# Performance work log

Measured on AMD Instinct MI355X. Metric: run time of the kernel, lower is better.

Reference implementation:

```python
import jax, jax.numpy as jnp
import numpy as np

N, E, B = 10000, 160000, 64
H, M, NE = 64, 64, 10
NIN = NE + 1
L = 16  # (max_ell+1)^2 spherical-harmonic components, max_ell=3
NUM_LAYERS = 2
AVG_NEIGH = 16.0
NORM = 4.0  # normalization_factor
EPS = 1e-9

silu = jax.nn.silu


def sph_harm(u):
    # component-normalized real spherical harmonics l=0..3 of unit vectors u [E,3]
    x, y, z = u[..., 0], u[..., 1], u[..., 2]
    xx, yy, zz = x * x, y * y, z * z
    return jnp.stack([
        jnp.ones_like(x),
        1.7320508 * x, 1.7320508 * y, 1.7320508 * z,
        3.8729833 * x * y, 3.8729833 * y * z, 1.1180340 * (3.0 * zz - 1.0),
        3.8729833 * x * z, 1.9364917 * (xx - yy),
        2.0916500 * y * (3.0 * xx - yy), 10.2469508 * x * y * z,
        1.6201852 * y * (5.0 * zz - 1.0), 1.3228757 * z * (5.0 * zz - 3.0),
        1.6201852 * x * (5.0 * zz - 1.0), 5.1234754 * (xx - yy) * z,
        2.0916500 * x * (xx - 3.0 * yy),
    ], axis=-1)


def setup_inputs() -> dict:
    key = jax.random.key(0)
    ks = jax.random.split(key, 24)
    inp = {}
    inp["positions"] = jax.random.normal(ks[0], (N, 3), jnp.float32) * 3.0
    inp["node_attrs"] = jax.random.uniform(ks[1], (N, NE), jnp.float32)
    inp["t"] = jax.random.uniform(ks[2], (B, 1), jnp.float32)
    inp["shifts"] = jnp.zeros((E, 3), jnp.float32)
    inp["batch"] = jnp.sort(jax.random.randint(ks[3], (N,), 0, B))
    inp["edge_index"] = jax.random.randint(ks[4], (2, E), 0, N)

    def w(k, shape, fan_in):
        return (jax.random.normal(k, shape, jnp.float32) / np.float32(np.sqrt(fan_in)))

    inp["W_emb"] = w(ks[5], (NIN, H), NIN)
    inp["b_emb"] = jnp.zeros((H,), jnp.float32)
    inp["W_out"] = w(ks[6], (H, NIN), H)
    inp["b_out"] = jnp.zeros((NIN,), jnp.float32)
    inp["Wr1"] = w(ks[7], (NUM_LAYERS, 1, H), 1)
    inp["br1"] = jnp.zeros((NUM_LAYERS, H), jnp.float32)
    inp["Wr2"] = w(ks[8], (NUM_LAYERS, H, H), H)
    inp["W_up"] = w(ks[9], (NUM_LAYERS, H, H), H)
    inp["W_mix"] = w(ks[10], (NUM_LAYERS, H, H), H)
    inp["W_prod"] = w(ks[11], (NUM_LAYERS, H, H), H)
    inp["Wro1"] = w(ks[12], (NUM_LAYERS, H, M), H)
    inp["bro1"] = jnp.zeros((NUM_LAYERS, M), jnp.float32)
    inp["Wro2"] = w(ks[13], (NUM_LAYERS, M, H), M)
    inp["Wg"] = w(ks[14], (NUM_LAYERS, H, H), H)
    inp["wv"] = w(ks[15], (NUM_LAYERS, H), H)
    inp["Wmlp1"] = w(ks[16], (NUM_LAYERS, 2 * H, H), 2 * H)
    inp["bmlp1"] = jnp.zeros((NUM_LAYERS, H), jnp.float32)
    inp["Wmlp2"] = w(ks[17], (NUM_LAYERS, H, H), H)
    inp["bmlp2"] = jnp.zeros((NUM_LAYERS, H), jnp.float32)
    return inp


def reference(positions, node_attrs, t, shifts, batch, edge_index,
              W_emb, b_emb, W_out, b_out,
              Wr1, br1, Wr2, W_up, W_mix, W_prod,
              Wro1, bro1, Wro2, Wg, wv,
              Wmlp1, bmlp1, Wmlp2, bmlp2):
    snd, rcv = edge_index[0], edge_index[1]

    def edges(p):
        v = p[rcv] - p[snd] + shifts          # [E,3]
        return v, jnp.linalg.norm(v, axis=-1, keepdims=True)

    na = node_attrs / NORM
    h = jnp.concatenate([na, t[batch]], axis=-1) @ W_emb + b_emb   # [N,H]
    nf = jnp.zeros((N, H, L), h.dtype).at[:, :, 0].set(h)          # scalars -> l=0 slot
    pos0 = positions
    pos = positions
    vec, lengths = edges(pos)

    for i in range(NUM_LAYERS):
        u = vec / (jnp.linalg.norm(vec, axis=-1, keepdims=True) + EPS)
        Y = sph_harm(u)                                            # [E,L]
        # radial MLP on edge lengths -> per-edge channel weights
        r = silu(lengths @ Wr1[i] + br1[i]) @ Wr2[i]               # [E,H]
        nf_up = jnp.einsum('nhl,hk->nkl', nf, W_up[i])             # channel mix (equivariant)
        # depthwise tensor product: (radial * sender scalar) x Y, then scatter-sum
        msg = (r * nf_up[snd, :, 0])[:, :, None] * Y[:, None, :]   # [E,H,L]
        agg = jax.ops.segment_sum(msg, rcv, num_segments=N) / AVG_NEIGH
        a = jnp.einsum('nhl,hk->nkl', agg, W_mix[i])
        # symmetric contraction (correlation=3): equivariant scalar-gated polynomial
        s = a[:, :, 0:1]
        nf = jnp.einsum('nhl,hk->nkl', a * (1.0 + s + s * s), W_prod[i])
        # nonlinear readout: scalar MLP + gated vector head
        sc = nf[:, :, 0]                                           # [N,H]
        v3 = nf[:, :, 1:4]                                         # [N,H,3]
        scalars = silu(sc @ Wro1[i] + bro1[i]) @ Wro2[i]           # [N,H]
        gate = silu(sc @ Wg[i])                                    # [N,H]
        vout = jnp.einsum('nhc,h->nc', v3 * gate[:, :, None], wv[i])  # [N,3]
        pos = pos + vout
        h = h + silu(jnp.concatenate([h, scalars], axis=-1) @ Wmlp1[i] + bmlp1[i]) @ Wmlp2[i] + bmlp2[i]
        vec, lengths = edges(pos)

    pred = h @ W_out + b_out                                       # [N,NIN]
    counts = jax.ops.segment_sum(jnp.ones((N, 1), pos.dtype), batch, num_segments=B)
    means = jax.ops.segment_sum(pos, batch, num_segments=B) / jnp.maximum(counts, 1.0)
    pred_pos = (pos - means[batch]) - pos0                         # remove_mean - positions_0
    return pred[:, :-1], pred_pos
```

## Files before the change

kernel.cpp:

```cpp
#include <hip/hip_runtime.h>

#define NN 10000
#define NEDGE 160000
#define NBATCH 64

static constexpr size_t OFF_POS   = 0;
static constexpr size_t OFF_H     = 30016;
static constexpr size_t OFF_NF0   = OFF_H   + 640000;
static constexpr size_t OFF_NUP   = OFF_NF0 + 640000;
static constexpr size_t OFF_V3    = OFF_NUP + 640000;
static constexpr size_t OFF_Q1    = OFF_V3  + 1920000;
static constexpr size_t OFF_AGG   = OFF_Q1  + 640000;
static constexpr size_t OFF_WW    = OFF_AGG + 2560000;
static constexpr size_t OFF_WY    = OFF_WW  + 10240000;
static constexpr size_t OFF_ESLOT = OFF_WY  + 640000;
static constexpr size_t OFF_CSR   = OFF_ESLOT + 160000;
static constexpr size_t OFF_CNT   = OFF_CSR + 10016;
static constexpr size_t OFF_CUR   = OFF_CNT + 10016;
static constexpr size_t OFF_BACC  = OFF_CUR + 10016;
static constexpr size_t WS_END    = OFF_BACC + 256;

__device__ __forceinline__ float silu_f(float x) {
  return x / (1.0f + __expf(-x));
}

__global__ __launch_bounds__(256) void k_embed_count_up(
    const float* __restrict__ pos_in, const float* __restrict__ na,
    const float* __restrict__ t, const int* __restrict__ batch,
    const float* __restrict__ Wemb, const float* __restrict__ bemb,
    const float* __restrict__ Wup0,
    float* __restrict__ h, float* __restrict__ nf0, float* __restrict__ pos_cur,
    float* __restrict__ nfup0,
    const int* __restrict__ ei, int* __restrict__ counts) {
  if (blockIdx.x >= 2500) {
    int e = (blockIdx.x - 2500) * 256 + threadIdx.x;
    atomicAdd(&counts[ei[NEDGE + e]], 1);
    return;
  }
  __shared__ float sx[4][64];
  int tid = blockIdx.x * 256 + threadIdx.x;
  int n = tid >> 6, k = tid & 63;
  int w = threadIdx.x >> 6;
  float acc = bemb[k];
  const float* arow = na + n * 10;
#pragma unroll
  for (int j = 0; j < 10; ++j)
    acc = fmaf(arow[j] * 0.25f, Wemb[j * 64 + k], acc);
  acc = fmaf(t[batch[n]], Wemb[10 * 64 + k], acc);
  h[tid] = acc;
  nf0[tid] = acc;
  if (k < 3) pos_cur[n * 3 + k] = pos_in[n * 3 + k];
  sx[w][k] = acc;
  __syncthreads();
  float up = 0.f;
  for (int hh = 0; hh < 64; ++hh)
    up = fmaf(sx[w][hh], Wup0[hh * 64 + k], up);
  nfup0[tid] = up;
}

__global__ __launch_bounds__(1024) void k_scan(const int* __restrict__ counts,
                                               int* __restrict__ offs) {
  __shared__ int part[1024];
  int tid = threadIdx.x;
  int base = tid * 10;
  int local[10];
  int s = 0;
#pragma unroll
  for (int j = 0; j < 10; ++j) {
    int idx = base + j;
    int v = (idx < NN) ? counts[idx] : 0;
    local[j] = s;
    s += v;
  }
  part[tid] = s;
  __syncthreads();
  for (int d = 1; d < 1024; d <<= 1) {
    int v = (tid >= d) ? part[tid - d] : 0;
    __syncthreads();
    part[tid] += v;
    __syncthreads();
  }
  int excl = (tid == 0) ? 0 : part[tid - 1];
#pragma unroll
  for (int j = 0; j < 10; ++j) {
    int idx = base + j;
    if (idx < NN) offs[idx] = excl + local[j];
  }
  if (tid == 1023) offs[NN] = excl + s;
}

__global__ __launch_bounds__(256) void k_scatter(
    const int* __restrict__ ei, const int* __restrict__ offs,
    int* __restrict__ cursor, int* __restrict__ eslot) {
  int e = blockIdx.x * 256 + threadIdx.x;
  int r = ei[NEDGE + e];
  int slot = atomicAdd(&cursor[r], 1);
  eslot[e] = offs[r] + slot;
}

__global__ __launch_bounds__(256) void k_edge(
    const int* __restrict__ ei, const float* __restrict__ shifts,
    const float* __restrict__ pos, const float* __restrict__ nfup0,
    const float* __restrict__ Wr1, const float* __restrict__ br1,
    const float* __restrict__ Wr2, const int* __restrict__ eslot,
    float* __restrict__ w_s, float4* __restrict__ y_s) {
  __shared__ float4 sW[1024];
  __shared__ float sW1[64];
  __shared__ float sB1[64];
  {
    const float4* W4 = (const float4*)Wr2;
    for (int i = threadIdx.x; i < 1024; i += 256) sW[i] = W4[i];
    if (threadIdx.x < 64) { sW1[threadIdx.x] = Wr1[threadIdx.x]; sB1[threadIdx.x] = br1[threadIdx.x]; }
  }
  __syncthreads();
  int wq   = threadIdx.x >> 6;
  int lane = threadIdx.x & 63;
  int ebase = blockIdx.x * 256 + lane * 4;

  float len[4]; int slot[4]; int snd[4];
#pragma unroll
  for (int q = 0; q < 4; ++q) {
    int e = ebase + q;
    int s = ei[e], r = ei[NEDGE + e];
    snd[q] = s;
    float vx = pos[r * 3 + 0] - pos[s * 3 + 0] + shifts[e * 3 + 0];
    float vy = pos[r * 3 + 1] - pos[s * 3 + 1] + shifts[e * 3 + 1];
    float vz = pos[r * 3 + 2] - pos[s * 3 + 2] + shifts[e * 3 + 2];
    float l = sqrtf(vx * vx + vy * vy + vz * vz);
    len[q] = l;
    slot[q] = eslot[e];
    if (wq == 0) {
      float inv = 1.0f / (l + 1e-9f);
      const float c1 = 1.7320508f * 0.0625f;
      y_s[slot[q]] = make_float4(0.0625f, c1 * vx * inv, c1 * vy * inv, c1 * vz * inv);
    }
  }

  float4 acc[4][4];
#pragma unroll
  for (int q = 0; q < 4; ++q)
#pragma unroll
    for (int j = 0; j < 4; ++j) acc[q][j] = make_float4(0.f, 0.f, 0.f, 0.f);

  const float4* sWq = sW + wq * 4;
  for (int hh = 0; hh < 64; ++hh) {
    float w1 = sW1[hh], b1 = sB1[hh];
    float sl[4];
#pragma unroll
    for (int q = 0; q < 4; ++q)
      sl[q] = silu_f(fmaf(len[q], w1, b1));
#pragma unroll
    for (int j = 0; j < 4; ++j) {
      float4 wv = sWq[hh * 16 + j];
#pragma unroll
      for (int q = 0; q < 4; ++q) {
        acc[q][j].x = fmaf(sl[q], wv.x, acc[q][j].x);
        acc[q][j].y = fmaf(sl[q], wv.y, acc[q][j].y);
        acc[q][j].z = fmaf(sl[q], wv.z, acc[q][j].z);
        acc[q][j].w = fmaf(sl[q], wv.w, acc[q][j].w);
      }
    }
  }

#pragma unroll
  for (int q = 0; q < 4; ++q) {
    const float4* nrow = (const float4*)(nfup0 + (size_t)snd[q] * 64) + wq * 4;
    float4* wrow = (float4*)(w_s + (size_t)slot[q] * 64) + wq * 4;
#pragma unroll
    for (int j = 0; j < 4; ++j) {
      float4 nv = nrow[j];
      float4 o;
      o.x = acc[q][j].x * nv.x; o.y = acc[q][j].y * nv.y;
      o.z = acc[q][j].z * nv.z; o.w = acc[q][j].w * nv.w;
      wrow[j] = o;
    }
  }
}

__global__ __launch_bounds__(256) void k_gather(
    const int* __restrict__ offs, const float* __restrict__ w_s,
    const float4* __restrict__ y_s, float4* __restrict__ agg) {
  int gtid = blockIdx.x * 256 + threadIdx.x;
  int n = gtid >> 6;
  int lane = threadIdx.x & 63;
  int beg = offs[n], end = offs[n + 1];
  float a0 = 0.f, a1 = 0.f, a2 = 0.f, a3 = 0.f;
  for (int j = beg; j < end; ++j) {
    float w = w_s[(size_t)j * 64 + lane];
    float4 y = y_s[j];
    a0 = fmaf(w, y.x, a0);
    a1 = fmaf(w, y.y, a1);
    a2 = fmaf(w, y.z, a2);
    a3 = fmaf(w, y.w, a3);
  }
  agg[(size_t)n * 64 + lane] = make_float4(a0, a1, a2, a3);
}

__global__ __launch_bounds__(512) void k_mix_prod(
    const float4* __restrict__ agg, const float* __restrict__ Wmix,
    const float* __restrict__ Wprod, float* __restrict__ nf0,
    float* __restrict__ v3, const float* __restrict__ Wup_next,
    float* __restrict__ nfup0) {
  __shared__ float sMix[4096];
  __shared__ float sProd[4096];
  __shared__ float sUp[4096];
  __shared__ float4 xb[8][64];
  for (int i = threadIdx.x; i < 4096; i += 512) { sMix[i] = Wmix[i]; sProd[i] = Wprod[i]; }
  if (Wup_next)
    for (int i = threadIdx.x; i < 4096; i += 512) sUp[i] = Wup_next[i];
  int w = threadIdx.x >> 6, lane = threadIdx.x & 63;
  __syncthreads();
  for (int it = 0; it < 5; ++it) {
    int n = it * 2000 + blockIdx.x * 8 + w;
    xb[w][lane] = agg[(size_t)n * 64 + lane];
    __syncthreads();
    float4 a = make_float4(0.f, 0.f, 0.f, 0.f);
    for (int hh = 0; hh < 64; ++hh) {
      float4 x = xb[w][hh];
      float m = sMix[hh * 64 + lane];
      a.x = fmaf(x.x, m, a.x); a.y = fmaf(x.y, m, a.y);
      a.z = fmaf(x.z, m, a.z); a.w = fmaf(x.w, m, a.w);
    }
    float sv = a.x;
    float f = 1.0f + sv + sv * sv;
    a.x *= f; a.y *= f; a.z *= f; a.w *= f;
    __syncthreads();
    xb[w][lane] = a;
    __syncthreads();
    float4 nf = make_float4(0.f, 0.f, 0.f, 0.f);
    for (int hh = 0; hh < 64; ++hh) {
      float4 x = xb[w][hh];
      float m = sProd[hh * 64 + lane];
      nf.x = fmaf(x.x, m, nf.x); nf.y = fmaf(x.y, m, nf.y);
      nf.z = fmaf(x.z, m, nf.z); nf.w = fmaf(x.w, m, nf.w);
    }
    nf0[(size_t)n * 64 + lane] = nf.x;
    v3[(size_t)n * 192 + lane * 3 + 0] = nf.y;
    v3[(size_t)n * 192 + lane * 3 + 1] = nf.z;
    v3[(size_t)n * 192 + lane * 3 + 2] = nf.w;
    if (Wup_next) {
      __syncthreads();
      xb[w][lane].x = nf.x;
      __syncthreads();
      float up = 0.f;
      for (int hh = 0; hh < 64; ++hh)
        up = fmaf(xb[w][hh].x, sUp[hh * 64 + lane], up);
      nfup0[(size_t)n * 64 + lane] = up;
    }
    __syncthreads();
  }
}

__global__ __launch_bounds__(512) void k_readout_mlp(
    const float* __restrict__ nf0, const float* __restrict__ v3,
    const float* __restrict__ Wro1, const float* __restrict__ bro1,
    const float* __restrict__ Wg, const float* __restrict__ wvv,
    const float* __restrict__ Wro2,
    const float* __restrict__ Wmlp1, const float* __restrict__ bmlp1,
    const float* __restrict__ Wmlp2, const float* __restrict__ bmlp2,
    float* __restrict__ pos, float* __restrict__ h) {
  __shared__ float sR[4096];
  __shared__ float sG[4096];
  __shared__ float sRo2[4096];
  __shared__ float sM1[8192];
  __shared__ float sM2[4096];
  __shared__ float sx[8][64], sq[8][64], ssc[8][64], sh[8][64], su[8][64];
  __shared__ float swv[64];
  for (int i = threadIdx.x; i < 4096; i += 512) {
    sR[i] = Wro1[i]; sG[i] = Wg[i]; sRo2[i] = Wro2[i]; sM2[i] = Wmlp2[i];
  }
  for (int i = threadIdx.x; i < 8192; i += 512) sM1[i] = Wmlp1[i];
  if (threadIdx.x < 64) swv[threadIdx.x] = wvv[threadIdx.x];
  int w = threadIdx.x >> 6, lane = threadIdx.x & 63;
  __syncthreads();
  for (int it = 0; it < 5; ++it) {
    int n = it * 2000 + blockIdx.x * 8 + w;
    sx[w][lane] = nf0[(size_t)n * 64 + lane];
    sh[w][lane] = h[(size_t)n * 64 + lane];
    __syncthreads();
    float q = bro1[lane];
    float g = 0.f;
    for (int hh = 0; hh < 64; ++hh) {
      float x = sx[w][hh];
      q = fmaf(x, sR[hh * 64 + lane], q);
      g = fmaf(x, sG[hh * 64 + lane], g);
    }
    q = silu_f(q);
    g = silu_f(g);
    float gw = g * swv[lane];
    float p0 = v3[(size_t)n * 192 + lane * 3 + 0] * gw;
    float p1 = v3[(size_t)n * 192 + lane * 3 + 1] * gw;
    float p2 = v3[(size_t)n * 192 + lane * 3 + 2] * gw;
#pragma unroll
    for (int m = 32; m > 0; m >>= 1) {
      p0 += __shfl_xor(p0, m);
      p1 += __shfl_xor(p1, m);
      p2 += __shfl_xor(p2, m);
    }
    if (lane == 0) {
      pos[n * 3 + 0] += p0;
      pos[n * 3 + 1] += p1;
      pos[n * 3 + 2] += p2;
    }
    sq[w][lane] = q;
    __syncthreads();
    float sc = 0.f;
    for (int m = 0; m < 64; ++m) sc = fmaf(sq[w][m], sRo2[m * 64 + lane], sc);
    ssc[w][lane] = sc;
    __syncthreads();
    float u = bmlp1[lane];
    for (int j = 0; j < 64; ++j) u = fmaf(sh[w][j], sM1[j * 64 + lane], u);
    for (int j = 0; j < 64; ++j) u = fmaf(ssc[w][j], sM1[(64 + j) * 64 + lane], u);
    u = silu_f(u);
    su[w][lane] = u;
    __syncthreads();
    float ho = sh[w][lane] + bmlp2[lane];
    for (int m = 0; m < 64; ++m) ho = fmaf(su[w][m], sM2[m * 64 + lane], ho);
    h[(size_t)n * 64 + lane] = ho;
    __syncthreads();
  }
}

__global__ __launch_bounds__(256) void k_pred(
    const float* __restrict__ h, const float* __restrict__ Wout,
    const float* __restrict__ bout, float* __restrict__ out) {
  __shared__ float sW[704];
  for (int i = threadIdx.x; i < 704; i += 256) sW[i] = Wout[i];
  __syncthreads();
  int n = blockIdx.x * 256 + threadIdx.x;
  if (n >= NN) return;
  float acc[10];
#pragma unroll
  for (int j = 0; j < 10; ++j) acc[j] = bout[j];
  const float* row = h + (size_t)n * 64;
  for (int hh = 0; hh < 64; ++hh) {
    float hv = row[hh];
#pragma unroll
    for (int j = 0; j < 10; ++j) acc[j] = fmaf(hv, sW[hh * 11 + j], acc[j]);
  }
  float* orow = out + (size_t)n * 10;
#pragma unroll
  for (int j = 0; j < 10; ++j) orow[j] = acc[j];
}

__global__ __launch_bounds__(256) void k_batch(
    const int* __restrict__ batch, const float* __restrict__ pos,
    float* __restrict__ bacc) {
  int n = blockIdx.x * 256 + threadIdx.x;
  int lane = threadIdx.x & 63;
  bool valid = n < NN;
  int b = valid ? batch[n] : -1;
  float p0 = valid ? pos[n * 3 + 0] : 0.f;
  float p1 = valid ? pos[n * 3 + 1] : 0.f;
  float p2 = valid ? pos[n * 3 + 2] : 0.f;
  float c  = valid ? 1.f : 0.f;
#pragma unroll
  for (int d = 1; d < 64; d <<= 1) {
    float q0 = __shfl_down(p0, d);
    float q1 = __shfl_down(p1, d);
    float q2 = __shfl_down(p2, d);
    float qc = __shfl_down(c, d);
    int bd   = __shfl_down(b, d);
    if (lane + d < 64 && bd == b) { p0 += q0; p1 += q1; p2 += q2; c += qc; }
  }
  int bprev = __shfl_up(b, 1);
  bool head = valid && (lane == 0 || bprev != b);
  if (head) {
    atomicAdd(&bacc[b * 4 + 0], p0);
    atomicAdd(&bacc[b * 4 + 1], p1);
    atomicAdd(&bacc[b * 4 + 2], p2);
    atomicAdd(&bacc[b * 4 + 3], c);
  }
}

__global__ __launch_bounds__(256) void k_predpos(
    const int* __restrict__ batch, const float* __restrict__ pos,
    const float* __restrict__ pos0, const float* __restrict__ bacc,
    float* __restrict__ out) {
  int n = blockIdx.x * 256 + threadIdx.x;
  if (n >= NN) return;
  int b = batch[n];
  float cnt = fmaxf(bacc[b * 4 + 3], 1.0f);
#pragma unroll
  for (int c = 0; c < 3; ++c)
    out[NN * 10 + n * 3 + c] = pos[n * 3 + c] - bacc[b * 4 + c] / cnt - pos0[n * 3 + c];
}

extern "C" void kernel_launch(void* const* d_in, const int* in_sizes, int n_in,
                              void* d_out, int out_size, void* d_ws, size_t ws_size,
                              hipStream_t stream) {
  const float* positions = (const float*)d_in[0];
  const float* node_attrs = (const float*)d_in[1];
  const float* t_in = (const float*)d_in[2];
  const float* shifts = (const float*)d_in[3];
  const int* batch = (const int*)d_in[4];
  const int* edge_index = (const int*)d_in[5];
  const float* W_emb = (const float*)d_in[6];
  const float* b_emb = (const float*)d_in[7];
  const float* W_out = (const float*)d_in[8];
  const float* b_out = (const float*)d_in[9];
  const float* Wr1 = (const float*)d_in[10];
  const float* br1 = (const float*)d_in[11];
  const float* Wr2 = (const float*)d_in[12];
  const float* W_up = (const float*)d_in[13];
  const float* W_mix = (const float*)d_in[14];
  const float* W_prod = (const float*)d_in[15];
  const float* Wro1 = (const float*)d_in[16];
  const float* bro1 = (const float*)d_in[17];
  const float* Wro2 = (const float*)d_in[18];
  const float* Wg = (const float*)d_in[19];
  const float* wv = (const float*)d_in[20];
  const float* Wmlp1 = (const float*)d_in[21];
  const float* bmlp1 = (const float*)d_in[22];
  const float* Wmlp2 = (const float*)d_in[23];
  const float* bmlp2 = (const float*)d_in[24];

  float* ws = (float*)d_ws;
  float* pos_cur = ws + OFF_POS;
  float* hbuf    = ws + OFF_H;
  float* nf0     = ws + OFF_NF0;
  float* nfup0   = ws + OFF_NUP;
  float* v3      = ws + OFF_V3;
  float4* agg    = (float4*)(ws + OFF_AGG);
  float* w_s     = ws + OFF_WW;
  float4* y_s    = (float4*)(ws + OFF_WY);
  int* eslot     = (int*)(ws + OFF_ESLOT);
  int* csroff    = (int*)(ws + OFF_CSR);
  int* counts    = (int*)(ws + OFF_CNT);
  int* cursor    = (int*)(ws + OFF_CUR);
  float* bacc    = ws + OFF_BACC;

  hipMemsetAsync(counts, 0, (WS_END - OFF_CNT) * sizeof(float), stream);

  k_embed_count_up<<<3125, 256, 0, stream>>>(positions, node_attrs, t_in, batch,
                                             W_emb, b_emb, W_up,
                                             hbuf, nf0, pos_cur, nfup0,
                                             edge_index, counts);
  k_scan<<<1, 1024, 0, stream>>>(counts, csroff);
  k_scatter<<<625, 256, 0, stream>>>(edge_index, csroff, cursor, eslot);

  for (int i = 0; i < 2; ++i) {
    k_edge<<<625, 256, 0, stream>>>(edge_index, shifts, pos_cur, nfup0,
                                    Wr1 + i * 64, br1 + i * 64, Wr2 + i * 4096,
                                    eslot, w_s, y_s);
    k_gather<<<2500, 256, 0, stream>>>(csroff, w_s, y_s, agg);
    k_mix_prod<<<250, 512, 0, stream>>>(agg, W_mix + i * 4096, W_prod + i * 4096,
                                        nf0, v3,
                                        (i == 0) ? (W_up + 4096) : nullptr, nfup0);
    k_readout_mlp<<<250, 512, 0, stream>>>(nf0, v3, Wro1 + i * 4096, bro1 + i * 64,
                                           Wg + i * 4096, wv + i * 64,
                                           Wro2 + i * 4096,
                                           Wmlp1 + i * 8192, bmlp1 + i * 64,
                                           Wmlp2 + i * 4096, bmlp2 + i * 64,
                                           pos_cur, hbuf);
  }

  k_pred<<<40, 256, 0, stream>>>(hbuf, W_out, b_out, (float*)d_out);
  k_batch<<<40, 256, 0, stream>>>(batch, pos_cur, bacc);
  k_predpos<<<40, 256, 0, stream>>>(batch, pos_cur, positions, bacc, (float*)d_out);
}
```

Measured before the change: 402.3 us.

## Register-tile node MLP kernels: each thread computes four output columns

Rewrites k_mix_prod and k_readout_mlp so that each thread owns four output columns of one node, reading float4 weights from shared memory. Each block now handles 16 nodes in a single pass over 625 blocks instead of looping five times over 8 nodes. This cuts shared-memory loads per FMA and removes most __syncthreads. Outputs are written as vectorized float4 stores, and the vector-head reduction shrinks to a 16-lane shuffle. The trade-off is that each block reloads the weight matrices into shared memory for only 16 nodes, and k_edge also gets a min-blocks occupancy hint.

```diff
diff --git a/kernel.cpp b/kernel.cpp
--- a/kernel.cpp
+++ b/kernel.cpp
@@ -98,7 +98,7 @@
   eslot[e] = offs[r] + slot;
 }
 
-__global__ __launch_bounds__(256) void k_edge(
+__global__ __launch_bounds__(256, 2) void k_edge(
     const int* __restrict__ ei, const float* __restrict__ shifts,
     const float* __restrict__ pos, const float* __restrict__ nfup0,
     const float* __restrict__ Wr1, const float* __restrict__ br1,
@@ -196,7 +196,7 @@
   agg[(size_t)n * 64 + lane] = make_float4(a0, a1, a2, a3);
 }
 
-__global__ __launch_bounds__(512) void k_mix_prod(
+__global__ __launch_bounds__(256) void k_mix_prod(
     const float4* __restrict__ agg, const float* __restrict__ Wmix,
     const float* __restrict__ Wprod, float* __restrict__ nf0,
     float* __restrict__ v3, const float* __restrict__ Wup_next,
@@ -204,54 +204,82 @@
   __shared__ float sMix[4096];
   __shared__ float sProd[4096];
   __shared__ float sUp[4096];
-  __shared__ float4 xb[8][64];
-  for (int i = threadIdx.x; i < 4096; i += 512) { sMix[i] = Wmix[i]; sProd[i] = Wprod[i]; }
+  __shared__ float4 xa[16][65];
+  for (int i = threadIdx.x; i < 4096; i += 256) { sMix[i] = Wmix[i]; sProd[i] = Wprod[i]; }
   if (Wup_next)
-    for (int i = threadIdx.x; i < 4096; i += 512) sUp[i] = Wup_next[i];
-  int w = threadIdx.x >> 6, lane = threadIdx.x & 63;
+    for (int i = threadIdx.x; i < 4096; i += 256) sUp[i] = Wup_next[i];
+  int nb = blockIdx.x * 16;
+  for (int i = threadIdx.x; i < 1024; i += 256)
+    xa[i >> 6][i & 63] = agg[(size_t)nb * 64 + i];
   __syncthreads();
-  for (int it = 0; it < 5; ++it) {
-    int n = it * 2000 + blockIdx.x * 8 + w;
-    xb[w][lane] = agg[(size_t)n * 64 + lane];
-    __syncthreads();
-    float4 a = make_float4(0.f, 0.f, 0.f, 0.f);
+
+  int lane = threadIdx.x & 63, w = threadIdx.x >> 6;
+  int q = lane >> 4, c16 = lane & 15;
+  int nloc = w * 4 + q;
+  int n = nb + nloc;
+  int col0 = c16 * 4;
+
+  float4 a0 = {0,0,0,0}, a1 = {0,0,0,0}, a2 = {0,0,0,0}, a3 = {0,0,0,0};
+  for (int hh = 0; hh < 64; ++hh) {
+    float4 xv = xa[nloc][hh];
+    float4 wm = *(const float4*)&sMix[hh * 64 + col0];
+    a0.x = fmaf(xv.x, wm.x, a0.x); a0.y = fmaf(xv.y, wm.x, a0.y);
+    a0.z = fmaf(xv.z, wm.x, a0.z); a0.w = fmaf(xv.w, wm.x, a0.w);
+    a1.x = fmaf(xv.x, wm.y, a1.x); a1.y = fmaf(xv.y, wm.y, a1.y);
+    a1.z = fmaf(xv.z, wm.y, a1.z); a1.w = fmaf(xv.w, wm.y, a1.w);
+    a2.x = fmaf(xv.x, wm.z, a2.x); a2.y = fmaf(xv.y, wm.z, a2.y);
+    a2.z = fmaf(xv.z, wm.z, a2.z); a2.w = fmaf(xv.w, wm.z, a2.w);
+    a3.x = fmaf(xv.x, wm.w, a3.x); a3.y = fmaf(xv.y, wm.w, a3.y);
+    a3.z = fmaf(xv.z, wm.w, a3.z); a3.w = fmaf(xv.w, wm.w, a3.w);
+  }
+  {
+    float s0 = a0.x, f0 = 1.0f + s0 + s0 * s0;
+    float s1 = a1.x, f1 = 1.0f + s1 + s1 * s1;
+    float s2 = a2.x, f2 = 1.0f + s2 + s2 * s2;
+    float s3 = a3.x, f3 = 1.0f + s3 + s3 * s3;
+    a0.x *= f0; a0.y *= f0; a0.z *= f0; a0.w *= f0;
+    a1.x *= f1; a1.y *= f1; a1.z *= f1; a1.w *= f1;
+    a2.x *= f2; a2.y *= f2; a2.z *= f2; a2.w *= f2;
+    a3.x *= f3; a3.y *= f3; a3.z *= f3; a3.w *= f3;
+  }
+  xa[nloc][col0 + 0] = a0; xa[nloc][col0 + 1] = a1;
+  xa[nloc][col0 + 2] = a2; xa[nloc][col0 + 3] = a3;
+
+  float4 p0 = {0,0,0,0}, p1 = {0,0,0,0}, p2 = {0,0,0,0}, p3 = {0,0,0,0};
+  for (int hh = 0; hh < 64; ++hh) {
+    float4 xv = xa[nloc][hh];
+    float4 wm = *(const float4*)&sProd[hh * 64 + col0];
+    p0.x = fmaf(xv.x, wm.x, p0.x); p0.y = fmaf(xv.y, wm.x, p0.y);
+    p0.z = fmaf(xv.z, wm.x, p0.z); p0.w = fmaf(xv.w, wm.x, p0.w);
+    p1.x = fmaf(xv.x, wm.y, p1.x); p1.y = fmaf(xv.y, wm.y, p1.y);
+    p1.z = fmaf(xv.z, wm.y, p1.z); p1.w = fmaf(xv.w, wm.y, p1.w);
+    p2.x = fmaf(xv.x, wm.z, p2.x); p2.y = fmaf(xv.y, wm.z, p2.y);
+    p2.z = fmaf(xv.z, wm.z, p2.z); p2.w = fmaf(xv.w, wm.z, p2.w);
+    p3.x = fmaf(xv.x, wm.w, p3.x); p3.y = fmaf(xv.y, wm.w, p3.y);
+    p3.z = fmaf(xv.z, wm.w, p3.z); p3.w = fmaf(xv.w, wm.w, p3.w);
+  }
+  *(float4*)&nf0[(size_t)n * 64 + col0] = make_float4(p0.x, p1.x, p2.x, p3.x);
+  {
+    float4* v3p = (float4*)&v3[(size_t)n * 192 + col0 * 3];
+    v3p[0] = make_float4(p0.y, p0.z, p0.w, p1.y);
+    v3p[1] = make_float4(p1.z, p1.w, p2.y, p2.z);
+    v3p[2] = make_float4(p2.w, p3.y, p3.z, p3.w);
+  }
+  if (Wup_next) {
+    xa[nloc][col0 + 0] = p0; xa[nloc][col0 + 1] = p1;
+    xa[nloc][col0 + 2] = p2; xa[nloc][col0 + 3] = p3;
+    float u0 = 0.f, u1 = 0.f, u2 = 0.f, u3 = 0.f;
     for (int hh = 0; hh < 64; ++hh) {
-      float4 x = xb[w][hh];
-      float m = sMix[hh * 64 + lane];
-      a.x = fmaf(x.x, m, a.x); a.y = fmaf(x.y, m, a.y);
-      a.z = fmaf(x.z, m, a.z); a.w = fmaf(x.w, m, a.w);
+      float xs = xa[nloc][hh].x;
+      float4 wu = *(const float4*)&sUp[hh * 64 + col0];
+      u0 = fmaf(xs, wu.x, u0); u1 = fmaf(xs, wu.y, u1);
+      u2 = fmaf(xs, wu.z, u2); u3 = fmaf(xs, wu.w, u3);
     }
-    float sv = a.x;
-    float f = 1.0f + sv + sv * sv;
-    a.x *= f; a.y *= f; a.z *= f; a.w *= f;
-    __syncthreads();
-    xb[w][lane] = a;
-    __syncthreads();
-    float4 nf = make_float4(0.f, 0.f, 0.f, 0.f);
-    for (int hh = 0; hh < 64; ++hh) {
-      float4 x = xb[w][hh];
-      float m = sProd[hh * 64 + lane];
-      nf.x = fmaf(x.x, m, nf.x); nf.y = fmaf(x.y, m, nf.y);
-      nf.z = fmaf(x.z, m, nf.z); nf.w = fmaf(x.w, m, nf.w);
-    }
-    nf0[(size_t)n * 64 + lane] = nf.x;
-    v3[(size_t)n * 192 + lane * 3 + 0] = nf.y;
-    v3[(size_t)n * 192 + lane * 3 + 1] = nf.z;
-    v3[(size_t)n * 192 + lane * 3 + 2] = nf.w;
-    if (Wup_next) {
-      __syncthreads();
-      xb[w][lane].x = nf.x;
-      __syncthreads();
-      float up = 0.f;
-      for (int hh = 0; hh < 64; ++hh)
-        up = fmaf(xb[w][hh].x, sUp[hh * 64 + lane], up);
-      nfup0[(size_t)n * 64 + lane] = up;
-    }
-    __syncthreads();
-  }
-}
-
-__global__ __launch_bounds__(512) void k_readout_mlp(
+    *(float4*)&nfup0[(size_t)n * 64 + col0] = make_float4(u0, u1, u2, u3);
+  }
+}
+
+__global__ __launch_bounds__(256) void k_readout_mlp(
     const float* __restrict__ nf0, const float* __restrict__ v3,
     const float* __restrict__ Wro1, const float* __restrict__ bro1,
     const float* __restrict__ Wg, const float* __restrict__ wvv,
@@ -264,61 +292,101 @@
   __shared__ float sRo2[4096];
   __shared__ float sM1[8192];
   __shared__ float sM2[4096];
-  __shared__ float sx[8][64], sq[8][64], ssc[8][64], sh[8][64], su[8][64];
-  __shared__ float swv[64];
-  for (int i = threadIdx.x; i < 4096; i += 512) {
+  __shared__ float xs[16][68];
+  __shared__ float xh[16][68];
+  __shared__ float xq[16][68];
+  for (int i = threadIdx.x; i < 4096; i += 256) {
     sR[i] = Wro1[i]; sG[i] = Wg[i]; sRo2[i] = Wro2[i]; sM2[i] = Wmlp2[i];
   }
-  for (int i = threadIdx.x; i < 8192; i += 512) sM1[i] = Wmlp1[i];
-  if (threadIdx.x < 64) swv[threadIdx.x] = wvv[threadIdx.x];
-  int w = threadIdx.x >> 6, lane = threadIdx.x & 63;
+  for (int i = threadIdx.x; i < 8192; i += 256) sM1[i] = Wmlp1[i];
+  int nb = blockIdx.x * 16;
+  for (int i = threadIdx.x; i < 1024; i += 256) {
+    xs[i >> 6][i & 63] = nf0[(size_t)nb * 64 + i];
+    xh[i >> 6][i & 63] = h[(size_t)nb * 64 + i];
+  }
   __syncthreads();
-  for (int it = 0; it < 5; ++it) {
-    int n = it * 2000 + blockIdx.x * 8 + w;
-    sx[w][lane] = nf0[(size_t)n * 64 + lane];
-    sh[w][lane] = h[(size_t)n * 64 + lane];
-    __syncthreads();
-    float q = bro1[lane];
-    float g = 0.f;
-    for (int hh = 0; hh < 64; ++hh) {
-      float x = sx[w][hh];
-      q = fmaf(x, sR[hh * 64 + lane], q);
-      g = fmaf(x, sG[hh * 64 + lane], g);
-    }
-    q = silu_f(q);
-    g = silu_f(g);
-    float gw = g * swv[lane];
-    float p0 = v3[(size_t)n * 192 + lane * 3 + 0] * gw;
-    float p1 = v3[(size_t)n * 192 + lane * 3 + 1] * gw;
-    float p2 = v3[(size_t)n * 192 + lane * 3 + 2] * gw;
-#pragma unroll
-    for (int m = 32; m > 0; m >>= 1) {
+
+  int lane = threadIdx.x & 63, w = threadIdx.x >> 6;
+  int q = lane >> 4, c16 = lane & 15;
+  int nloc = w * 4 + q;
+  int n = nb + nloc;
+  int col0 = c16 * 4;
+
+  float qa0 = 0, qa1 = 0, qa2 = 0, qa3 = 0;
+  float ga0 = 0, ga1 = 0, ga2 = 0, ga3 = 0;
+  for (int m = 0; m < 64; ++m) {
+    float x = xs[nloc][m];
+    float4 wr = *(const float4*)&sR[m * 64 + col0];
+    float4 wg = *(const float4*)&sG[m * 64 + col0];
+    qa0 = fmaf(x, wr.x, qa0); qa1 = fmaf(x, wr.y, qa1);
+    qa2 = fmaf(x, wr.z, qa2); qa3 = fmaf(x, wr.w, qa3);
+    ga0 = fmaf(x, wg.x, ga0); ga1 = fmaf(x, wg.y, ga1);
+    ga2 = fmaf(x, wg.z, ga2); ga3 = fmaf(x, wg.w, ga3);
+  }
+  float4 b1v = *(const float4*)&bro1[col0];
+  float q0 = silu_f(qa0 + b1v.x), q1 = silu_f(qa1 + b1v.y);
+  float q2 = silu_f(qa2 + b1v.z), q3 = silu_f(qa3 + b1v.w);
+  float g0 = silu_f(ga0), g1 = silu_f(ga1), g2 = silu_f(ga2), g3 = silu_f(ga3);
+
+  {
+    float4 wv4 = *(const float4*)&wvv[col0];
+    const float4* v3p = (const float4*)&v3[(size_t)n * 192 + col0 * 3];
+    float4 va = v3p[0], vb = v3p[1], vc = v3p[2];
+    float gw0 = g0 * wv4.x, gw1 = g1 * wv4.y, gw2 = g2 * wv4.z, gw3 = g3 * wv4.w;
+    float p0 = va.x * gw0 + va.w * gw1 + vb.z * gw2 + vc.y * gw3;
+    float p1 = va.y * gw0 + vb.x * gw1 + vb.w * gw2 + vc.z * gw3;
+    float p2 = va.z * gw0 + vb.y * gw1 + vc.x * gw2 + vc.w * gw3;
+#pragma unroll
+    for (int m = 1; m < 16; m <<= 1) {
       p0 += __shfl_xor(p0, m);
       p1 += __shfl_xor(p1, m);
       p2 += __shfl_xor(p2, m);
     }
-    if (lane == 0) {
+    if (c16 == 0) {
       pos[n * 3 + 0] += p0;
       pos[n * 3 + 1] += p1;
       pos[n * 3 + 2] += p2;
     }
-    sq[w][lane] = q;
-    __syncthreads();
-    float sc = 0.f;
-    for (int m = 0; m < 64; ++m) sc = fmaf(sq[w][m], sRo2[m * 64 + lane], sc);
-    ssc[w][lane] = sc;
-    __syncthreads();
-    float u = bmlp1[lane];
-    for (int j = 0; j < 64; ++j) u = fmaf(sh[w][j], sM1[j * 64 + lane], u);
-    for (int j = 0; j < 64; ++j) u = fmaf(ssc[w][j], sM1[(64 + j) * 64 + lane], u);
-    u = silu_f(u);
-    su[w][lane] = u;
-    __syncthreads();
-    float ho = sh[w][lane] + bmlp2[lane];
-    for (int m = 0; m < 64; ++m) ho = fmaf(su[w][m], sM2[m * 64 + lane], ho);
-    h[(size_t)n * 64 + lane] = ho;
-    __syncthreads();
-  }
+  }
+
+  *(float4*)&xq[nloc][col0] = make_float4(q0, q1, q2, q3);
+  float s20 = 0, s21 = 0, s22 = 0, s23 = 0;
+  for (int m = 0; m < 64; ++m) {
+    float x = xq[nloc][m];
+    float4 w2 = *(const float4*)&sRo2[m * 64 + col0];
+    s20 = fmaf(x, w2.x, s20); s21 = fmaf(x, w2.y, s21);
+    s22 = fmaf(x, w2.z, s22); s23 = fmaf(x, w2.w, s23);
+  }
+  *(float4*)&xs[nloc][col0] = make_float4(s20, s21, s22, s23);
+
+  float4 bm1 = *(const float4*)&bmlp1[col0];
+  float u0 = bm1.x, u1 = bm1.y, u2 = bm1.z, u3 = bm1.w;
+  for (int m = 0; m < 64; ++m) {
+    float xm = xh[nloc][m];
+    float4 m1 = *(const float4*)&sM1[m * 64 + col0];
+    u0 = fmaf(xm, m1.x, u0); u1 = fmaf(xm, m1.y, u1);
+    u2 = fmaf(xm, m1.z, u2); u3 = fmaf(xm, m1.w, u3);
+  }
+  for (int m = 0; m < 64; ++m) {
+    float xm = xs[nloc][m];
+    float4 m1 = *(const float4*)&sM1[(64 + m) * 64 + col0];
+    u0 = fmaf(xm, m1.x, u0); u1 = fmaf(xm, m1.y, u1);
+    u2 = fmaf(xm, m1.z, u2); u3 = fmaf(xm, m1.w, u3);
+  }
+  u0 = silu_f(u0); u1 = silu_f(u1); u2 = silu_f(u2); u3 = silu_f(u3);
+  *(float4*)&xq[nloc][col0] = make_float4(u0, u1, u2, u3);
+
+  float4 bm2 = *(const float4*)&bmlp2[col0];
+  float4 hold = *(float4*)&xh[nloc][col0];
+  float h0 = hold.x + bm2.x, h1 = hold.y + bm2.y;
+  float h2 = hold.z + bm2.z, h3 = hold.w + bm2.w;
+  for (int m = 0; m < 64; ++m) {
+    float um = xq[nloc][m];
+    float4 m2 = *(const float4*)&sM2[m * 64 + col0];
+    h0 = fmaf(um, m2.x, h0); h1 = fmaf(um, m2.y, h1);
+    h2 = fmaf(um, m2.z, h2); h3 = fmaf(um, m2.w, h3);
+  }
+  *(float4*)&h[(size_t)n * 64 + col0] = make_float4(h0, h1, h2, h3);
 }
 
 __global__ __launch_bounds__(256) void k_pred(
@@ -444,10 +512,10 @@
                                     Wr1 + i * 64, br1 + i * 64, Wr2 + i * 4096,
                                     eslot, w_s, y_s);
     k_gather<<<2500, 256, 0, stream>>>(csroff, w_s, y_s, agg);
-    k_mix_prod<<<250, 512, 0, stream>>>(agg, W_mix + i * 4096, W_prod + i * 4096,
+    k_mix_prod<<<625, 256, 0, stream>>>(agg, W_mix + i * 4096, W_prod + i * 4096,
                                         nf0, v3,
                                         (i == 0) ? (W_up + 4096) : nullptr, nfup0);
-    k_readout_mlp<<<250, 512, 0, stream>>>(nf0, v3, Wro1 + i * 4096, bro1 + i * 64,
+    k_readout_mlp<<<625, 256, 0, stream>>>(nf0, v3, Wro1 + i * 4096, bro1 + i * 64,
                                            Wg + i * 4096, wv + i * 64,
                                            Wro2 + i * 4096,
                                            Wmlp1 + i * 8192, bmlp1 + i * 64,
```

New measurement: 389.0 us. 1.03x faster.
